# Optimization experiments

Hardware: AMD Instinct MI355X
Metric: run time of the kernel (lower is better)

The kernel has to match this reference:

```python
import math
import jax, jax.numpy as jnp
import numpy as np

B, T, H, A, F = 2, 2048, 2048, 2048, 8192
L, LID, EPS = 24, 0, 1e-5
NEG_INF = -1e38


def setup_inputs() -> dict:
    key = jax.random.key(0)
    ks = jax.random.split(key, 8)
    s = 0.02
    # RWKV init-derived time parameters for layer_id=0, num_hidden_layers=24
    ratio_0_to_1 = LID / (L - 1)          # 0.0
    ratio_1_to_almost_0 = 1.0 - LID / L    # 1.0
    x = jnp.arange(H, dtype=jnp.float32) / H
    tmk = jnp.power(x, ratio_1_to_almost_0)
    tmv = tmk + 0.3 * ratio_0_to_1
    tmr = jnp.power(x, 0.5 * ratio_1_to_almost_0)
    zigzag = 0.5 * (jnp.arange(1, A + 1, dtype=jnp.float32) % 3 - 1)
    time_first = jnp.full((A,), math.log(0.3), dtype=jnp.float32) + zigzag
    h = jnp.arange(A, dtype=jnp.float32)
    time_decay = -5.0 + 8.0 * (h / (A - 1)) ** (0.7 + 1.3 * ratio_0_to_1)
    return {
        'hidden': jax.random.normal(ks[0], (B, T, H), jnp.float32),
        'pre_w': jnp.ones((H,), jnp.float32), 'pre_b': jnp.zeros((H,), jnp.float32),
        'ln1_w': jnp.ones((H,), jnp.float32), 'ln1_b': jnp.zeros((H,), jnp.float32),
        'ln2_w': jnp.ones((H,), jnp.float32), 'ln2_b': jnp.zeros((H,), jnp.float32),
        'time_decay': time_decay, 'time_first': time_first,
        'tmk': tmk, 'tmv': tmv, 'tmr': tmr,
        'Wk': jax.random.normal(ks[1], (H, A), jnp.float32) * s,
        'Wv': jax.random.normal(ks[2], (H, A), jnp.float32) * s,
        'Wr': jax.random.normal(ks[3], (H, A), jnp.float32) * s,
        'Wo': jax.random.normal(ks[4], (A, H), jnp.float32) * s,
        'f_tmk': jnp.power(x, ratio_1_to_almost_0), 'f_tmr': jnp.power(x, ratio_1_to_almost_0),
        'f_Wk': jax.random.normal(ks[5], (H, F), jnp.float32) * s,
        'f_Wr': jax.random.normal(ks[6], (H, H), jnp.float32) * s,
        'f_Wv': jax.random.normal(ks[7], (F, H), jnp.float32) * s,
    }


def _ln(x, w, b):
    mu = x.mean(-1, keepdims=True)
    var = ((x - mu) ** 2).mean(-1, keepdims=True)
    return (x - mu) * jax.lax.rsqrt(var + EPS) * w + b


def _token_shift(x):
    # sx state is zeros at init: prepend a zero row, drop the last token
    return jnp.concatenate((jnp.zeros_like(x[:, :1, :]), x[:, :-1, :]), axis=1)


def _forward(hidden, pre_w, pre_b, ln1_w, ln1_b, ln2_w, ln2_b,
             time_decay, time_first, tmk, tmv, tmr, Wk, Wv, Wr, Wo,
             f_tmk, f_tmr, f_Wk, f_Wr, f_Wv):
    h0 = _ln(hidden, pre_w, pre_b)          # pre_ln (layer_id == 0)
    # ---- time mixing (RwkvSelfAttention) ----
    x1 = _ln(h0, ln1_w, ln1_b)
    cx = _token_shift(x1)
    kx = x1 * tmk + cx * (1 - tmk)
    vx = x1 * tmv + cx * (1 - tmv)
    rx = x1 * tmr + cx * (1 - tmr)
    r = jax.nn.sigmoid(rx @ Wr)             # [B,T,A]
    k = kx @ Wk
    v = vx @ Wv
    w_decay = -jnp.exp(time_decay)          # [A]

    def step(carry, kv):
        aa, bb, pp = carry                  # each [B,A]
        kk, vv = kv                         # each [B,A]
        ww = time_first + kk
        q = jnp.maximum(pp, ww)
        e1 = jnp.exp(pp - q)
        e2 = jnp.exp(ww - q)
        out = (e1 * aa + e2 * vv) / (e1 * bb + e2)
        ww2 = w_decay + pp
        q2 = jnp.maximum(ww2, kk)
        e1 = jnp.exp(ww2 - q2)
        e2 = jnp.exp(kk - q2)
        return (e1 * aa + e2 * vv, e1 * bb + e2, q2), out

    init = (jnp.zeros((B, A), k.dtype), jnp.zeros((B, A), k.dtype),
            jnp.full((B, A), NEG_INF, jnp.float32))
    _, wkv = jax.lax.scan(step, init, (jnp.swapaxes(k, 0, 1), jnp.swapaxes(v, 0, 1)))
    wkv = jnp.swapaxes(wkv, 0, 1)           # [B,T,A]
    h1 = h0 + (r * wkv) @ Wo
    # ---- channel mixing (RwkvFeedForward) ----
    x2 = _ln(h1, ln2_w, ln2_b)
    cx2 = _token_shift(x2)
    kx2 = x2 * f_tmk + cx2 * (1 - f_tmk)
    rx2 = x2 * f_tmr + cx2 * (1 - f_tmr)
    r2 = jax.nn.sigmoid(rx2 @ f_Wr)
    kk2 = jnp.square(jax.nn.relu(kx2 @ f_Wk))
    return h1 + r2 * (kk2 @ f_Wv)


def reference(hidden, pre_w, pre_b, ln1_w, ln1_b, ln2_w, ln2_b,
              time_decay, time_first, tmk, tmv, tmr, Wk, Wv, Wr, Wo,
              f_tmk, f_tmr, f_Wk, f_Wr, f_Wv):
    return _forward(hidden, pre_w, pre_b, ln1_w, ln1_b, ln2_w, ln2_b,
                    time_decay, time_first, tmk, tmv, tmr, Wk, Wv, Wr, Wo,
                    f_tmk, f_tmr, f_Wk, f_Wr, f_Wv)
```

## Files before the change

kernel.cpp:

```cpp
#include <hip/hip_runtime.h>

#define B_  2
#define T_  2048
#define H_  2048
#define A_  2048
#define F_  8192
#define BT_ 4096

typedef __bf16  bf16x8 __attribute__((ext_vector_type(8)));
typedef float   f32x4  __attribute__((ext_vector_type(4)));
typedef short   short8 __attribute__((ext_vector_type(8)));

__device__ __forceinline__ float bf2f(unsigned short b) {
  return __uint_as_float(((unsigned)b) << 16);
}
__device__ __forceinline__ unsigned short f2bf(float f) {
  unsigned u = __float_as_uint(f);
  unsigned r = (u + 0x7FFFu + ((u >> 16) & 1u)) >> 16;
  return (unsigned short)r;
}

typedef __attribute__((address_space(3))) void lds_void_t;
typedef __attribute__((address_space(1))) const void gc_void_t;
__device__ __forceinline__ void gload_lds16(const void* g, void* l) {
  __builtin_amdgcn_global_load_lds((gc_void_t*)g, (lds_void_t*)l, 16, 0, 0);
}

__global__ void canary_kernel(float* out) { out[threadIdx.x] = 1000.0f; }

__global__ __launch_bounds__(256) void transpose_bf16_kernel(
    const float* __restrict__ src, unsigned short* __restrict__ dst, int Kd, int Nd)
{
  __shared__ float tile[32][33];
  const int tx = threadIdx.x & 31;
  const int ty = threadIdx.x >> 5;
  const int n0 = blockIdx.x * 32;
  const int k0 = blockIdx.y * 32;
#pragma unroll
  for (int i = 0; i < 32; i += 8)
    tile[ty + i][tx] = src[(size_t)(k0 + ty + i) * Nd + n0 + tx];
  __syncthreads();
#pragma unroll
  for (int i = 0; i < 32; i += 8)
    dst[(size_t)(n0 + ty + i) * Kd + k0 + tx] = f2bf(tile[tx][ty + i]);
}

__device__ __forceinline__ void block_reduce2(float& a, float& b) {
#pragma unroll
  for (int off = 32; off > 0; off >>= 1) {
    a += __shfl_down(a, off, 64);
    b += __shfl_down(b, off, 64);
  }
  __shared__ float sa[4], sb[4];
  const int lane = threadIdx.x & 63, w = threadIdx.x >> 6;
  __syncthreads();
  if (lane == 0) { sa[w] = a; sb[w] = b; }
  __syncthreads();
  a = sa[0] + sa[1] + sa[2] + sa[3];
  b = sb[0] + sb[1] + sb[2] + sb[3];
}

__global__ __launch_bounds__(256) void ln_pre_kernel(
    const float* __restrict__ hidden,
    const float* __restrict__ pw, const float* __restrict__ pb,
    const float* __restrict__ w1, const float* __restrict__ b1,
    float* __restrict__ h0, unsigned short* __restrict__ x1)
{
  const int row = blockIdx.x, tid = threadIdx.x;
  const int c0 = tid * 8;
  const size_t base = (size_t)row * H_ + c0;
  float x[8];
  float4 v0 = *(const float4*)(hidden + base);
  float4 v1 = *(const float4*)(hidden + base + 4);
  x[0]=v0.x; x[1]=v0.y; x[2]=v0.z; x[3]=v0.w;
  x[4]=v1.x; x[5]=v1.y; x[6]=v1.z; x[7]=v1.w;
  float s = 0.f, s2 = 0.f;
#pragma unroll
  for (int j = 0; j < 8; ++j) { s += x[j]; s2 += x[j]*x[j]; }
  block_reduce2(s, s2);
  float mu  = s * (1.f / H_);
  float inv = rsqrtf(fmaxf(s2 * (1.f / H_) - mu*mu, 0.f) + 1e-5f);
  float y[8];
#pragma unroll
  for (int j = 0; j < 8; ++j) y[j] = (x[j] - mu) * inv * pw[c0+j] + pb[c0+j];
  *(float4*)(h0 + base)     = make_float4(y[0],y[1],y[2],y[3]);
  *(float4*)(h0 + base + 4) = make_float4(y[4],y[5],y[6],y[7]);
  s = 0.f; s2 = 0.f;
#pragma unroll
  for (int j = 0; j < 8; ++j) { s += y[j]; s2 += y[j]*y[j]; }
  block_reduce2(s, s2);
  mu  = s * (1.f / H_);
  inv = rsqrtf(fmaxf(s2 * (1.f / H_) - mu*mu, 0.f) + 1e-5f);
  unsigned o[4];
#pragma unroll
  for (int p = 0; p < 4; ++p) {
    unsigned lo = f2bf((y[2*p]   - mu) * inv * w1[c0+2*p]   + b1[c0+2*p]);
    unsigned hi = f2bf((y[2*p+1] - mu) * inv * w1[c0+2*p+1] + b1[c0+2*p+1]);
    o[p] = lo | (hi << 16);
  }
  *(uint4*)(x1 + base) = make_uint4(o[0], o[1], o[2], o[3]);
}

__global__ __launch_bounds__(256) void lnmix2_kernel(
    const float* __restrict__ h1,
    const float* __restrict__ w_, const float* __restrict__ b_,
    const float* __restrict__ tmk_, const float* __restrict__ tmr_,
    unsigned short* __restrict__ kx2b, unsigned short* __restrict__ rx2b)
{
  const int row = blockIdx.x, tid = threadIdx.x;
  const int t = row & (T_ - 1);
  const int c0 = tid * 8;
  const size_t base = (size_t)row * H_ + c0;
  float x[8], p[8];
  {
    float4 v0 = *(const float4*)(h1 + base);
    float4 v1 = *(const float4*)(h1 + base + 4);
    x[0]=v0.x; x[1]=v0.y; x[2]=v0.z; x[3]=v0.w;
    x[4]=v1.x; x[5]=v1.y; x[6]=v1.z; x[7]=v1.w;
  }
  const bool hasp = (t > 0);
  if (hasp) {
    float4 v0 = *(const float4*)(h1 + base - H_);
    float4 v1 = *(const float4*)(h1 + base - H_ + 4);
    p[0]=v0.x; p[1]=v0.y; p[2]=v0.z; p[3]=v0.w;
    p[4]=v1.x; p[5]=v1.y; p[6]=v1.z; p[7]=v1.w;
  } else {
#pragma unroll
    for (int j = 0; j < 8; ++j) p[j] = 0.f;
  }
  float s = 0.f, s2 = 0.f;
#pragma unroll
  for (int j = 0; j < 8; ++j) { s += x[j]; s2 += x[j]*x[j]; }
  block_reduce2(s, s2);
  const float mu  = s * (1.f / H_);
  const float inv = rsqrtf(fmaxf(s2 * (1.f / H_) - mu*mu, 0.f) + 1e-5f);
  float sp = 0.f, sp2 = 0.f;
#pragma unroll
  for (int j = 0; j < 8; ++j) { sp += p[j]; sp2 += p[j]*p[j]; }
  block_reduce2(sp, sp2);
  const float mup  = sp * (1.f / H_);
  const float invp = rsqrtf(fmaxf(sp2 * (1.f / H_) - mup*mup, 0.f) + 1e-5f);
  unsigned ok[4], orr[4];
#pragma unroll
  for (int q = 0; q < 4; ++q) {
    unsigned ko = 0, ro = 0;
#pragma unroll
    for (int h = 0; h < 2; ++h) {
      const int j = q*2 + h;
      const float xr = (x[j] - mu) * inv * w_[c0+j] + b_[c0+j];
      const float cr = hasp ? (p[j] - mup) * invp * w_[c0+j] + b_[c0+j] : 0.f;
      ko |= (unsigned)f2bf(fmaf(xr - cr, tmk_[c0+j], cr)) << (h*16);
      ro |= (unsigned)f2bf(fmaf(xr - cr, tmr_[c0+j], cr)) << (h*16);
    }
    ok[q] = ko; orr[q] = ro;
  }
  *(uint4*)(kx2b + base) = make_uint4(ok[0],ok[1],ok[2],ok[3]);
  *(uint4*)(rx2b + base) = make_uint4(orr[0],orr[1],orr[2],orr[3]);
}

__global__ __launch_bounds__(256) void mix1_kernel(
    const unsigned short* __restrict__ x,
    const float* __restrict__ tm_,
    unsigned short* __restrict__ outb)
{
  const int row = blockIdx.x;
  const int t = row & (T_ - 1);
  const int c0 = threadIdx.x * 8;
  const size_t base = (size_t)row * H_ + c0;
  uint4 xv = *(const uint4*)(x + base);
  uint4 cv = make_uint4(0u,0u,0u,0u);
  if (t > 0) cv = *(const uint4*)(x + base - H_);
  const unsigned xs[4] = {xv.x, xv.y, xv.z, xv.w};
  const unsigned cs[4] = {cv.x, cv.y, cv.z, cv.w};
  unsigned oo[4];
#pragma unroll
  for (int p = 0; p < 4; ++p) {
    unsigned w = 0;
#pragma unroll
    for (int h = 0; h < 2; ++h) {
      const int j = p*2 + h;
      float xf = bf2f((unsigned short)((xs[p] >> (h*16)) & 0xFFFFu));
      float cf = bf2f((unsigned short)((cs[p] >> (h*16)) & 0xFFFFu));
      w |= (unsigned)f2bf(fmaf(xf - cf, tm_[c0+j], cf)) << (h*16);
    }
    oo[p] = w;
  }
  *(uint4*)(outb + base) = make_uint4(oo[0],oo[1],oo[2],oo[3]);
}

#define WKV_G 32
#define WKV_C 32
#define WKV_L 64

__global__ __launch_bounds__(1024) void wkv_scan_kernel(
    const unsigned short* __restrict__ kg, const unsigned short* __restrict__ vg,
    const unsigned short* __restrict__ rg,
    const float* __restrict__ time_first, const float* __restrict__ time_decay,
    unsigned short* __restrict__ rwkv)
{
  const int tid = threadIdx.x;
  const int al  = tid & (WKV_G - 1);
  const int c   = tid >> 5;
  const int b   = blockIdx.x >> 6;
  const int ag  = blockIdx.x & 63;
  const int a   = ag * WKV_G + al;
  const float tf = time_first[a];
  const float w  = -__expf(time_decay[a]);
  const size_t cb = (size_t)b * T_ * A_ + a + (size_t)c * WKV_L * A_;

  float aa = 0.f, bb = 0.f, pp = -1e38f;
  {
    float kb[4], vb[4];
#pragma unroll
    for (int j = 0; j < 4; ++j) {
      kb[j] = bf2f(kg[cb + (size_t)j * A_]);
      vb[j] = bf2f(vg[cb + (size_t)j * A_]);
    }
    for (int t0 = 0; t0 < WKV_L; t0 += 4) {
#pragma unroll
      for (int j = 0; j < 4; ++j) {
        const float kk = kb[j], vv = vb[j];
        const int tn = t0 + j + 4;
        if (tn < WKV_L) {
          kb[j] = bf2f(kg[cb + (size_t)tn * A_]);
          vb[j] = bf2f(vg[cb + (size_t)tn * A_]);
        }
        float ww2 = w + pp;
        float q2  = fmaxf(ww2, kk);
        float e1  = __expf(ww2 - q2);
        float e2  = __expf(kk  - q2);
        aa = e1*aa + e2*vv;
        bb = e1*bb + e2;
        pp = q2;
      }
    }
  }
  __shared__ float saa[WKV_C][WKV_G], sbb[WKV_C][WKV_G], spp[WKV_C][WKV_G];
  saa[c][al] = aa; sbb[c][al] = bb; spp[c][al] = pp;
  __syncthreads();

  if (tid < WKV_G) {
    float Aa = 0.f, Bb = 0.f, Pp = -1e38f;
    const float Lw = (float)WKV_L * w;
    for (int cc = 0; cc < WKV_C; ++cc) {
      const float na = saa[cc][tid], nb = sbb[cc][tid], np = spp[cc][tid];
      saa[cc][tid] = Aa; sbb[cc][tid] = Bb; spp[cc][tid] = Pp;
      const float p1 = Pp + Lw;
      const float pc = fmaxf(p1, np);
      const float f1 = __expf(p1 - pc);
      const float f2 = __expf(np - pc);
      Aa = f1*Aa + f2*na;
      Bb = f1*Bb + f2*nb;
      Pp = pc;
    }
  }
  __syncthreads();
  aa = saa[c][al]; bb = sbb[c][al]; pp = spp[c][al];

  {
    float kb[4], vb[4], rb[4];
#pragma unroll
    for (int j = 0; j < 4; ++j) {
      kb[j] = bf2f(kg[cb + (size_t)j * A_]);
      vb[j] = bf2f(vg[cb + (size_t)j * A_]);
      rb[j] = bf2f(rg[cb + (size_t)j * A_]);
    }
    for (int t0 = 0; t0 < WKV_L; t0 += 4) {
#pragma unroll
      for (int j = 0; j < 4; ++j) {
        const float kk = kb[j], vv = vb[j], rr = rb[j];
        const int tn = t0 + j + 4;
        if (tn < WKV_L) {
          kb[j] = bf2f(kg[cb + (size_t)tn * A_]);
          vb[j] = bf2f(vg[cb + (size_t)tn * A_]);
          rb[j] = bf2f(rg[cb + (size_t)tn * A_]);
        }
        float ww = tf + kk;
        float q  = fmaxf(pp, ww);
        float e1 = __expf(pp - q);
        float e2 = __expf(ww - q);
        float o  = (e1*aa + e2*vv) / (e1*bb + e2);
        float sr = 1.f / (1.f + __expf(-rr));
        rwkv[cb + (size_t)(t0 + j) * A_] = f2bf(sr * o);
        float ww2 = w + pp;
        float q2  = fmaxf(ww2, kk);
        e1 = __expf(ww2 - q2);
        e2 = __expf(kk  - q2);
        aa = e1*aa + e2*vv;
        bb = e1*bb + e2;
        pp = q2;
      }
    }
  }
}

enum { EPI_BF16 = 0, EPI_ADDIP = 1, EPI_RELU2 = 2, EPI_SIGADD = 3 };

template <int BM, int NBUF, int RG, int CG, int EPI>
__global__ __launch_bounds__(512) void gemm4_kernel(
    const unsigned short* __restrict__ Ap, const unsigned short* __restrict__ Bp,
    void* __restrict__ Cp, int K, int Nn,
    const unsigned short* __restrict__ sigb)
{
  constexpr int BN = 256;
  constexpr int FM = BM / 32;
  constexpr int FN = 4;
  __shared__ unsigned short As[NBUF * BM * 64];
  __shared__ unsigned short Bs[NBUF * BN * 64];
  const int tid  = threadIdx.x;
  const int lane = tid & 63;
  const int lr = lane & 15;
  const int hi = lane >> 4;
  const int rx7 = lr & 7;
  const int wid = tid >> 6;
  const int wm = wid >> 2, wn = wid & 3;
  const int rowW = wm * (BM / 2);
  const int colW = wn * 64;
  const int gx = gridDim.x;
  const int gy = gridDim.y;
  const int flat = blockIdx.y * gx + blockIdx.x;
  const int xcd = flat & 7;
  const int j = flat >> 3;
  const int rgc = gy / RG;
  const int r_idx = xcd % rgc;
  const int c_idx = xcd / rgc;
  const int row_l = j % RG;
  const int col_l = j / RG;
  const long row0 = (long)(r_idx * RG + row_l) * BM;
  const long col0 = (long)(c_idx * CG + col_l) * BN;
  const unsigned short* Ab = Ap + (size_t)row0 * K;
  const unsigned short* Bb = Bp + (size_t)col0 * K;
  const int srow8 = tid >> 3;
  const int sslot = (tid & 7) ^ (srow8 & 7);
  f32x4 acc[FM][FN] = {};

  auto SP0 = [&](int bufi, int tt) {
    unsigned short* asb = As + bufi * (BM * 64);
    unsigned short* bsb = Bs + bufi * (BN * 64);
    const size_t ko = (size_t)tt * 64 + sslot * 8;
    if constexpr (BM == 128) {
      gload_lds16(Ab + (size_t)srow8        * K + ko, asb + tid * 8);
      gload_lds16(Ab + (size_t)(srow8 + 64) * K + ko, asb + 4096 + tid * 8);
      gload_lds16(Bb + (size_t)srow8        * K + ko, bsb + tid * 8);
    } else {
      gload_lds16(Ab + (size_t)srow8         * K + ko, asb + tid * 8);
      gload_lds16(Ab + (size_t)(srow8 + 64)  * K + ko, asb + 4096  + tid * 8);
      gload_lds16(Ab + (size_t)(srow8 + 128) * K + ko, asb + 8192  + tid * 8);
      gload_lds16(Ab + (size_t)(srow8 + 192) * K + ko, asb + 12288 + tid * 8);
    }
  };
  auto SP1 = [&](int bufi, int tt) {
    unsigned short* bsb = Bs + bufi * (BN * 64);
    const size_t ko = (size_t)tt * 64 + sslot * 8;
    if constexpr (BM == 128) {
      gload_lds16(Bb + (size_t)(srow8 + 64)  * K + ko, bsb + 4096  + tid * 8);
      gload_lds16(Bb + (size_t)(srow8 + 128) * K + ko, bsb + 8192  + tid * 8);
      gload_lds16(Bb + (size_t)(srow8 + 192) * K + ko, bsb + 12288 + tid * 8);
    } else {
      gload_lds16(Bb + (size_t)srow8         * K + ko, bsb + tid * 8);
      gload_lds16(Bb + (size_t)(srow8 + 64)  * K + ko, bsb + 4096  + tid * 8);
      gload_lds16(Bb + (size_t)(srow8 + 128) * K + ko, bsb + 8192  + tid * 8);
      gload_lds16(Bb + (size_t)(srow8 + 192) * K + ko, bsb + 12288 + tid * 8);
    }
  };

  const int nt = K >> 6;
  SP0(0, 0); SP1(0, 0);
  if constexpr (NBUF == 3) { SP0(1, 1); SP1(1, 1); }
  int cur = 0;
  for (int t = 0; t < nt; ++t) {
    if constexpr (NBUF == 3) {
      if (t + 1 < nt) asm volatile("s_waitcnt vmcnt(6)" ::: "memory");
      else            asm volatile("s_waitcnt vmcnt(0)" ::: "memory");
    } else {
      asm volatile("s_waitcnt vmcnt(0)" ::: "memory");
    }
    __builtin_amdgcn_s_barrier();
    int nb = cur + (NBUF - 1); if (nb >= NBUF) nb -= NBUF;
    const unsigned short* asb = As + cur * (BM * 64);
    const unsigned short* bsb = Bs + cur * (BN * 64);
#pragma unroll
    for (int kk = 0; kk < 2; ++kk) {
      bf16x8 af[FM], bfr[FN];
#pragma unroll
      for (int m = 0; m < FM; ++m) {
        const int row = rowW + m*16 + lr;
        const int ps = (kk*4 + hi) ^ rx7;
        af[m] = __builtin_bit_cast(bf16x8, *(const short8*)(asb + row*64 + ps*8));
      }
#pragma unroll
      for (int n = 0; n < FN; ++n) {
        const int row = colW + n*16 + lr;
        const int ps = (kk*4 + hi) ^ rx7;
        bfr[n] = __builtin_bit_cast(bf16x8, *(const short8*)(bsb + row*64 + ps*8));
      }
      if (t + NBUF - 1 < nt) { if (kk == 0) SP0(nb, t + NBUF - 1); else SP1(nb, t + NBUF - 1); }
      asm volatile("s_waitcnt lgkmcnt(0)" ::: "memory");
      __builtin_amdgcn_sched_barrier(0);
      __builtin_amdgcn_s_setprio(1);
#pragma unroll
      for (int m = 0; m < FM; ++m)
#pragma unroll
        for (int n = 0; n < FN; ++n)
          acc[m][n] = __builtin_amdgcn_mfma_f32_16x16x32_bf16(af[m], bfr[n], acc[m][n], 0, 0, 0);
      __builtin_amdgcn_s_setprio(0);
      if (kk == 0) __builtin_amdgcn_s_barrier();
    }
    cur = (cur + 1 == NBUF) ? 0 : cur + 1;
  }

#pragma unroll
  for (int m = 0; m < FM; ++m) {
#pragma unroll
    for (int n = 0; n < FN; ++n) {
      const long col = col0 + colW + n*16 + lr;
#pragma unroll
      for (int j2 = 0; j2 < 4; ++j2) {
        const long row = row0 + rowW + m*16 + hi*4 + j2;
        const size_t idx = (size_t)row * Nn + col;
        const float v = acc[m][n][j2];
        if (EPI == EPI_BF16) {
          ((unsigned short*)Cp)[idx] = f2bf(v);
        } else if (EPI == EPI_ADDIP) {
          float* C = (float*)Cp;
          C[idx] = C[idx] + v;
        } else if (EPI == EPI_RELU2) {
          float rr = v > 0.f ? v : 0.f;
          ((unsigned short*)Cp)[idx] = f2bf(rr * rr);
        } else {
          float s = 1.f / (1.f + __expf(-bf2f(sigb[idx])));
          float* C = (float*)Cp;
          C[idx] = C[idx] + s * v;
        }
      }
    }
  }
}

#define MB(x) ((size_t)(x) << 20)
#define WS_NEED MB(184)

extern "C" void kernel_launch(void* const* d_in, const int* in_sizes, int n_in,
                              void* d_out, int out_size, void* d_ws, size_t ws_size,
                              hipStream_t stream) {
  const float* hidden     = (const float*)d_in[0];
  const float* pre_w      = (const float*)d_in[1];
  const float* pre_b      = (const float*)d_in[2];
  const float* ln1_w      = (const float*)d_in[3];
  const float* ln1_b      = (const float*)d_in[4];
  const float* ln2_w      = (const float*)d_in[5];
  const float* ln2_b      = (const float*)d_in[6];
  const float* time_decay = (const float*)d_in[7];
  const float* time_first = (const float*)d_in[8];
  const float* tmk        = (const float*)d_in[9];
  const float* tmv        = (const float*)d_in[10];
  const float* tmr        = (const float*)d_in[11];
  const float* Wk         = (const float*)d_in[12];
  const float* Wv         = (const float*)d_in[13];
  const float* Wr         = (const float*)d_in[14];
  const float* Wo         = (const float*)d_in[15];
  const float* f_tmk      = (const float*)d_in[16];
  const float* f_tmr      = (const float*)d_in[17];
  const float* f_Wk       = (const float*)d_in[18];
  const float* f_Wr       = (const float*)d_in[19];
  const float* f_Wv       = (const float*)d_in[20];
  float* out = (float*)d_out;
  char*  ws  = (char*)d_ws;

  if (ws_size < WS_NEED) {
    canary_kernel<<<1, 256, 0, stream>>>(out);
    return;
  }

  unsigned short* fWkT = (unsigned short*)(ws + MB(0));
  unsigned short* fWvT = (unsigned short*)(ws + MB(32));
  unsigned short* WkT  = (unsigned short*)(ws + MB(64));
  unsigned short* WvT  = (unsigned short*)(ws + MB(72));
  unsigned short* WrT  = (unsigned short*)(ws + MB(80));
  unsigned short* WoT  = (unsigned short*)(ws + MB(88));
  unsigned short* fWrT = (unsigned short*)(ws + MB(96));
  unsigned short* KK   = (unsigned short*)(ws + MB(64));
  unsigned short* S1   = (unsigned short*)(ws + MB(104));
  unsigned short* S4   = (unsigned short*)(ws + MB(120));
  unsigned short* S2   = (unsigned short*)(ws + MB(136));
  unsigned short* S3   = (unsigned short*)(ws + MB(152));
  unsigned short* M1   = (unsigned short*)(ws + MB(168));

  const dim3 blk(256);
  const dim3 blk512(512);
  const dim3 gSmall(8, 32);
  const dim3 gRelu(32, 16);

  transpose_bf16_kernel<<<dim3(64, 64),  blk, 0, stream>>>(Wk,   WkT,  2048, 2048);
  transpose_bf16_kernel<<<dim3(64, 64),  blk, 0, stream>>>(Wv,   WvT,  2048, 2048);
  transpose_bf16_kernel<<<dim3(64, 64),  blk, 0, stream>>>(Wr,   WrT,  2048, 2048);
  transpose_bf16_kernel<<<dim3(64, 64),  blk, 0, stream>>>(Wo,   WoT,  2048, 2048);
  transpose_bf16_kernel<<<dim3(64, 64),  blk, 0, stream>>>(f_Wr, fWrT, 2048, 2048);
  transpose_bf16_kernel<<<dim3(256, 64), blk, 0, stream>>>(f_Wk, fWkT, 2048, 8192);
  transpose_bf16_kernel<<<dim3(64, 256), blk, 0, stream>>>(f_Wv, fWvT, 8192, 2048);

  ln_pre_kernel<<<BT_, blk, 0, stream>>>(hidden, pre_w, pre_b, ln1_w, ln1_b, out, S1);

  mix1_kernel<<<BT_, blk, 0, stream>>>(S1, tmk, M1);
  gemm4_kernel<128,3,8,4,EPI_BF16><<<gSmall, blk512, 0, stream>>>(M1, WkT, S2, 2048, 2048, nullptr);
  mix1_kernel<<<BT_, blk, 0, stream>>>(S1, tmv, M1);
  gemm4_kernel<128,3,8,4,EPI_BF16><<<gSmall, blk512, 0, stream>>>(M1, WvT, S3, 2048, 2048, nullptr);
  mix1_kernel<<<BT_, blk, 0, stream>>>(S1, tmr, M1);
  gemm4_kernel<128,3,8,4,EPI_BF16><<<gSmall, blk512, 0, stream>>>(M1, WrT, S4, 2048, 2048, nullptr);

  wkv_scan_kernel<<<dim3(128), dim3(1024), 0, stream>>>(S2, S3, S4, time_first, time_decay, S1);

  gemm4_kernel<128,3,8,4,EPI_ADDIP><<<gSmall, blk512, 0, stream>>>(S1, WoT, out, 2048, 2048, nullptr);

  lnmix2_kernel<<<BT_, blk, 0, stream>>>(out, ln2_w, ln2_b, f_tmk, f_tmr, M1, S2);

  gemm4_kernel<128,3,8,4,EPI_BF16><<<gSmall, blk512, 0, stream>>>(S2, fWrT, S3, 2048, 2048, nullptr);

  gemm4_kernel<256,2,8,8,EPI_RELU2><<<gRelu, blk512, 0, stream>>>(M1, fWkT, KK, 2048, 8192, nullptr);

  gemm4_kernel<128,3,8,4,EPI_SIGADD><<<gSmall, blk512, 0, stream>>>(KK, fWvT, out, 8192, 2048, S3);
}
```

Baseline: 708.6 us.

## Split BM=256 GEMM main loop into four sub-steps with interleaved prefetch

For the 256-row tile variant, the K-step is split into four sub-steps (two k-halves times two M-halves). Each sub-step issues one quarter of the next tile's global-to-LDS loads, reuses the B fragments across both M-halves, and holds fewer A fragments in registers at a time. The mid-iteration barrier after the first k-half is removed for both variants. The goal is finer overlap of loads with MFMA work and lower register pressure. Dropping the barrier risks a race if the buffer indexing does not guarantee that writes to the next buffer cannot clobber data still being read.

```diff
diff --git a/kernel.cpp b/kernel.cpp
--- a/kernel.cpp
+++ b/kernel.cpp
@@ -338,35 +338,39 @@
     unsigned short* asb = As + bufi * (BM * 64);
     unsigned short* bsb = Bs + bufi * (BN * 64);
     const size_t ko = (size_t)tt * 64 + sslot * 8;
-    if constexpr (BM == 128) {
-      gload_lds16(Ab + (size_t)srow8        * K + ko, asb + tid * 8);
-      gload_lds16(Ab + (size_t)(srow8 + 64) * K + ko, asb + 4096 + tid * 8);
-      gload_lds16(Bb + (size_t)srow8        * K + ko, bsb + tid * 8);
-    } else {
-      gload_lds16(Ab + (size_t)srow8         * K + ko, asb + tid * 8);
-      gload_lds16(Ab + (size_t)(srow8 + 64)  * K + ko, asb + 4096  + tid * 8);
-      gload_lds16(Ab + (size_t)(srow8 + 128) * K + ko, asb + 8192  + tid * 8);
-      gload_lds16(Ab + (size_t)(srow8 + 192) * K + ko, asb + 12288 + tid * 8);
-    }
+    gload_lds16(Ab + (size_t)srow8        * K + ko, asb + tid * 8);
+    gload_lds16(Ab + (size_t)(srow8 + 64) * K + ko, asb + 4096 + tid * 8);
+    gload_lds16(Bb + (size_t)srow8        * K + ko, bsb + tid * 8);
   };
   auto SP1 = [&](int bufi, int tt) {
     unsigned short* bsb = Bs + bufi * (BN * 64);
     const size_t ko = (size_t)tt * 64 + sslot * 8;
-    if constexpr (BM == 128) {
-      gload_lds16(Bb + (size_t)(srow8 + 64)  * K + ko, bsb + 4096  + tid * 8);
-      gload_lds16(Bb + (size_t)(srow8 + 128) * K + ko, bsb + 8192  + tid * 8);
-      gload_lds16(Bb + (size_t)(srow8 + 192) * K + ko, bsb + 12288 + tid * 8);
+    gload_lds16(Bb + (size_t)(srow8 + 64)  * K + ko, bsb + 4096  + tid * 8);
+    gload_lds16(Bb + (size_t)(srow8 + 128) * K + ko, bsb + 8192  + tid * 8);
+    gload_lds16(Bb + (size_t)(srow8 + 192) * K + ko, bsb + 12288 + tid * 8);
+  };
+  auto SPq = [&](int bufi, int tt, int q) {
+    const size_t ko = (size_t)tt * 64 + sslot * 8;
+    if (q < 2) {
+      unsigned short* asb = As + bufi * (BM * 64);
+      gload_lds16(Ab + (size_t)(srow8 + q*128)      * K + ko, asb + q*8192 + tid * 8);
+      gload_lds16(Ab + (size_t)(srow8 + q*128 + 64) * K + ko, asb + q*8192 + 4096 + tid * 8);
     } else {
-      gload_lds16(Bb + (size_t)srow8         * K + ko, bsb + tid * 8);
-      gload_lds16(Bb + (size_t)(srow8 + 64)  * K + ko, bsb + 4096  + tid * 8);
-      gload_lds16(Bb + (size_t)(srow8 + 128) * K + ko, bsb + 8192  + tid * 8);
-      gload_lds16(Bb + (size_t)(srow8 + 192) * K + ko, bsb + 12288 + tid * 8);
+      const int qq = q - 2;
+      unsigned short* bsb = Bs + bufi * (BN * 64);
+      gload_lds16(Bb + (size_t)(srow8 + qq*128)      * K + ko, bsb + qq*8192 + tid * 8);
+      gload_lds16(Bb + (size_t)(srow8 + qq*128 + 64) * K + ko, bsb + qq*8192 + 4096 + tid * 8);
     }
   };
 
   const int nt = K >> 6;
-  SP0(0, 0); SP1(0, 0);
-  if constexpr (NBUF == 3) { SP0(1, 1); SP1(1, 1); }
+  if constexpr (BM == 128) {
+    SP0(0, 0); SP1(0, 0);
+    if constexpr (NBUF == 3) { SP0(1, 1); SP1(1, 1); }
+  } else {
+#pragma unroll
+    for (int q = 0; q < 4; ++q) SPq(0, 0, q);
+  }
   int cur = 0;
   for (int t = 0; t < nt; ++t) {
     if constexpr (NBUF == 3) {
@@ -379,32 +383,64 @@
     int nb = cur + (NBUF - 1); if (nb >= NBUF) nb -= NBUF;
     const unsigned short* asb = As + cur * (BM * 64);
     const unsigned short* bsb = Bs + cur * (BN * 64);
-#pragma unroll
-    for (int kk = 0; kk < 2; ++kk) {
-      bf16x8 af[FM], bfr[FN];
-#pragma unroll
-      for (int m = 0; m < FM; ++m) {
-        const int row = rowW + m*16 + lr;
-        const int ps = (kk*4 + hi) ^ rx7;
-        af[m] = __builtin_bit_cast(bf16x8, *(const short8*)(asb + row*64 + ps*8));
+    if constexpr (BM == 128) {
+#pragma unroll
+      for (int kk = 0; kk < 2; ++kk) {
+        bf16x8 af[4], bfr[4];
+#pragma unroll
+        for (int m = 0; m < 4; ++m) {
+          const int row = rowW + m*16 + lr;
+          const int ps = (kk*4 + hi) ^ rx7;
+          af[m] = __builtin_bit_cast(bf16x8, *(const short8*)(asb + row*64 + ps*8));
+        }
+#pragma unroll
+        for (int n = 0; n < 4; ++n) {
+          const int row = colW + n*16 + lr;
+          const int ps = (kk*4 + hi) ^ rx7;
+          bfr[n] = __builtin_bit_cast(bf16x8, *(const short8*)(bsb + row*64 + ps*8));
+        }
+        if (t + NBUF - 1 < nt) { if (kk == 0) SP0(nb, t + NBUF - 1); else SP1(nb, t + NBUF - 1); }
+        asm volatile("s_waitcnt lgkmcnt(0)" ::: "memory");
+        __builtin_amdgcn_sched_barrier(0);
+        __builtin_amdgcn_s_setprio(1);
+#pragma unroll
+        for (int m = 0; m < 4; ++m)
+#pragma unroll
+          for (int n = 0; n < 4; ++n)
+            acc[m][n] = __builtin_amdgcn_mfma_f32_16x16x32_bf16(af[m], bfr[n], acc[m][n], 0, 0, 0);
+        __builtin_amdgcn_s_setprio(0);
       }
-#pragma unroll
-      for (int n = 0; n < FN; ++n) {
-        const int row = colW + n*16 + lr;
-        const int ps = (kk*4 + hi) ^ rx7;
-        bfr[n] = __builtin_bit_cast(bf16x8, *(const short8*)(bsb + row*64 + ps*8));
+    } else {
+      bf16x8 bfrk[4];
+#pragma unroll
+      for (int sub = 0; sub < 4; ++sub) {
+        const int kk = sub >> 1, mh = sub & 1;
+        bf16x8 af[4];
+#pragma unroll
+        for (int m = 0; m < 4; ++m) {
+          const int row = rowW + (mh*4 + m)*16 + lr;
+          const int ps = (kk*4 + hi) ^ rx7;
+          af[m] = __builtin_bit_cast(bf16x8, *(const short8*)(asb + row*64 + ps*8));
+        }
+        if (mh == 0) {
+#pragma unroll
+          for (int n = 0; n < 4; ++n) {
+            const int row = colW + n*16 + lr;
+            const int ps = (kk*4 + hi) ^ rx7;
+            bfrk[n] = __builtin_bit_cast(bf16x8, *(const short8*)(bsb + row*64 + ps*8));
+          }
+        }
+        if (t + 1 < nt) SPq(nb, t + 1, sub);
+        asm volatile("s_waitcnt lgkmcnt(0)" ::: "memory");
+        __builtin_amdgcn_sched_barrier(0);
+        __builtin_amdgcn_s_setprio(1);
+#pragma unroll
+        for (int m = 0; m < 4; ++m)
+#pragma unroll
+          for (int n = 0; n < 4; ++n)
+            acc[mh*4 + m][n] = __builtin_amdgcn_mfma_f32_16x16x32_bf16(af[m], bfrk[n], acc[mh*4 + m][n], 0, 0, 0);
+        __builtin_amdgcn_s_setprio(0);
       }
-      if (t + NBUF - 1 < nt) { if (kk == 0) SP0(nb, t + NBUF - 1); else SP1(nb, t + NBUF - 1); }
-      asm volatile("s_waitcnt lgkmcnt(0)" ::: "memory");
-      __builtin_amdgcn_sched_barrier(0);
-      __builtin_amdgcn_s_setprio(1);
-#pragma unroll
-      for (int m = 0; m < FM; ++m)
-#pragma unroll
-        for (int n = 0; n < FN; ++n)
-          acc[m][n] = __builtin_amdgcn_mfma_f32_16x16x32_bf16(af[m], bfr[n], acc[m][n], 0, 0, 0);
-      __builtin_amdgcn_s_setprio(0);
-      if (kk == 0) __builtin_amdgcn_s_barrier();
     }
     cur = (cur + 1 == NBUF) ? 0 : cur + 1;
   }
```

Result: no change. 703.6 us (-0.7%).
